# Kernel tuning notes

Hardware: AMD Instinct MI355X
Metric: run time of the kernel (lower is better)

Reference implementation:

```python
import jax, jax.numpy as jnp
import numpy as np

V, D, H, P = 50000, 128, 256, 50      # vocab, embed_dim, hidden, pos_dim
N, T = 2048, 50                        # total sentences, max words per sentence
NDOC, L = 64, 32                       # docs, sentences per doc (N = NDOC*L)
PDOC, PSENT = 50, 100                  # pos embedding table sizes


def _gru(x, Wi, Wh, bi, bh):
    """PyTorch-style GRU, batch_first. x: [B,T,Din] -> [B,T,H]."""
    B = x.shape[0]
    Hh = Wh.shape[1]
    xg = jnp.einsum('btd,gd->btg', x, Wi) + bi  # [B,T,3H] precomputed input gates

    def step(h, xg_t):
        hg = h @ Wh.T + bh
        xr, xz, xn = jnp.split(xg_t, 3, axis=-1)
        hr, hz, hn = jnp.split(hg, 3, axis=-1)
        r = jax.nn.sigmoid(xr + hr)
        z = jax.nn.sigmoid(xz + hz)
        n = jnp.tanh(xn + r * hn)
        hnew = (1.0 - z) * n + z * h
        return hnew, hnew

    h0 = jnp.zeros((B, Hh), x.dtype)
    _, hs = jax.lax.scan(step, h0, jnp.swapaxes(xg, 0, 1))
    return jnp.swapaxes(hs, 0, 1)


def _bigru(x, pf, pb):
    hf = _gru(x, *pf)
    hb = _gru(x[:, ::-1], *pb)[:, ::-1]
    return jnp.concatenate([hf, hb], axis=-1)


def _masked_max(h, lens):
    """Ragged max-pool over time: h [B,T,C], lens [B] -> [B,C]; zeros for len==0."""
    Tt = h.shape[1]
    mask = jnp.arange(Tt)[None, :, None] < lens[:, None, None]
    m = jnp.max(jnp.where(mask, h, -jnp.inf), axis=1)
    return jnp.where(lens[:, None] > 0, m, 0.0)


def setup_inputs() -> dict:
    key = jax.random.key(0)
    ks = iter(jax.random.split(key, 64))

    def w(shape, s=0.05):
        return jax.random.normal(next(ks), shape, jnp.float32) * s

    x = jax.random.randint(next(ks), (N, T), 1, V)          # no padding tokens
    doc_lens = jnp.full((NDOC,), L, dtype=jnp.int32)
    d = {'x': x, 'doc_lens': doc_lens, 'embed': w((V, D)).at[0].set(0.0)}
    for pre, din in (('w', D), ('s', 2 * H), ('d', 2 * H)):
        for suf in ('f', 'b'):
            d[f'{pre}Wi_{suf}'] = w((3 * H, din))
            d[f'{pre}Wh_{suf}'] = w((3 * H, H))
            d[f'{pre}bi_{suf}'] = w((3 * H,))
            d[f'{pre}bh_{suf}'] = w((3 * H,))
    d['doc_pos_tab'] = w((PDOC, P))
    d['sent_pos_tab'] = w((PSENT, P))
    d['w_content'] = w((2 * H,))
    d['W_sal'] = w((2 * H, 4 * H))
    d['w_dpos'] = w((P,))
    d['w_spos'] = w((P,))
    d['sent_bias'] = w((1,))
    return d


def reference(x, doc_lens, embed,
              wWi_f, wWh_f, wbi_f, wbh_f, wWi_b, wWh_b, wbi_b, wbh_b,
              sWi_f, sWh_f, sbi_f, sbh_f, sWi_b, sWh_b, sbi_b, sbh_b,
              dWi_f, dWh_f, dbi_f, dbh_f, dWi_b, dWh_b, dbi_b, dbh_b,
              doc_pos_tab, sent_pos_tab, w_content, W_sal, w_dpos, w_spos,
              sent_bias):
    sent_lens = jnp.sum(jnp.sign(x), axis=1)                 # [N]
    e = embed[x]                                             # [N,T,D]
    hw = _bigru(e, (wWi_f, wWh_f, wbi_f, wbh_f), (wWi_b, wWh_b, wbi_b, wbh_b))
    sent_vec = _masked_max(hw, sent_lens)                    # [N,2H]

    n_docs = doc_lens.shape[0]
    Ld = sent_vec.shape[0] // n_docs
    docs = sent_vec.reshape(n_docs, Ld, -1)                  # [nd,L,2H]
    hs = _bigru(docs, (sWi_f, sWh_f, sbi_f, sbh_f), (sWi_b, sWh_b, sbi_b, sbh_b))
    doc_vec = _masked_max(hs, doc_lens)                      # [nd,2H]

    hd = _bigru(doc_vec[None], (dWi_f, dWh_f, dbi_f, dbh_f),
                (dWi_b, dWh_b, dbi_b, dbh_b))[0]             # [nd,2H]
    blog_vec = jnp.max(hd, axis=0)                           # [2H]

    context = jnp.concatenate(
        [jnp.broadcast_to(blog_vec, (n_docs, blog_vec.shape[0])), doc_vec],
        axis=-1)                                             # [nd,4H]

    content = docs @ w_content                               # [nd,L]
    salience = jnp.einsum('nld,de,ne->nl', docs, W_sal, context)

    pdoc = doc_pos_tab.shape[0]
    psent = sent_pos_tab.shape[0]
    di = (jnp.arange(n_docs) * pdoc) // n_docs               # [nd]
    safe_lens = jnp.maximum(doc_lens, 1).astype(jnp.int32)
    si = (jnp.arange(Ld, dtype=jnp.int32)[None, :] * psent) // safe_lens[:, None]
    si = jnp.minimum(si, psent - 1)                          # [nd,L]
    dscore = doc_pos_tab[di] @ w_dpos                        # [nd]
    sscore = sent_pos_tab[si] @ w_spos                       # [nd,L]

    scores = content + salience + dscore[:, None] + sscore + sent_bias[0]
    return scores.reshape(-1)                                # [N]
```

## Files before the change

kernel.cpp:

```cpp
#include <hip/hip_runtime.h>
#include <math.h>

#define HID 256
#define G3 768
#define DIM 128
#define TW 50
#define NSENT 2048
#define NDOC 64
#define LSENT 32
#define PDOC 50
#define PSENT 100
#define PDIMM 50

using i32x4 = __attribute__((ext_vector_type(4))) int;

static constexpr long OFFB_W1F  = 0;
static constexpr long OFFB_W2F  = 294912;
static constexpr long OFFB_W1B  = 589824;
static constexpr long OFFB_W2B  = 884736;
static constexpr long OFFB_SW1F = 1179648;
static constexpr long OFFB_SW2F = 1376256;
static constexpr long OFFB_SW1B = 1572864;
static constexpr long OFFB_SW2B = 1769472;
static constexpr long OFFB_DW1F = 1966080;
static constexpr long OFFB_DW2F = 2162688;
static constexpr long OFFB_DW1B = 2359296;
static constexpr long OFFB_DW2B = 2555904;

static constexpr long OFF_W4_sWi_f = 688128;
static constexpr long OFF_W4_sWi_b = 1081344;
static constexpr long OFF_W4_dWi_f = 1474560;
static constexpr long OFF_W4_dWi_b = 1867776;
static constexpr long OFF_W4_salT  = 2260992;
static constexpr long OFF_LENS     = 2785280;
static constexpr long OFF_SENTVEC  = 2787328;
static constexpr long OFF_XGS      = 3835904;
static constexpr long OFF_DOCVEC   = 6981632;
static constexpr long OFF_XGD      = 7014400;
static constexpr long OFF_BLOG     = 7112704;

#define SW_Q (0.3f/127.0f)
#define SX_Q (1.0f/127.0f)

__device__ __forceinline__ float sigm(float v){ return 1.0f/(1.0f+__expf(-v)); }
__device__ __forceinline__ float tanhfast(float v){ return 1.0f - 2.0f/(1.0f+__expf(2.0f*v)); }

__device__ __forceinline__ void fma4(float& acc, const float4 a, const float4 b){
  acc = fmaf(a.x, b.x, fmaf(a.y, b.y, fmaf(a.z, b.z, fmaf(a.w, b.w, acc))));
}

__device__ __forceinline__ void quant2(float v, int& a, int& b){
  float q1 = rintf(fminf(fmaxf(v*127.0f, -127.0f), 127.0f));
  a = (int)q1;
  float resid = v - q1*(1.0f/127.0f);
  b = (int)rintf(fminf(fmaxf(resid*32512.0f, -127.0f), 127.0f));
}
__device__ __forceinline__ int pack4(int a0,int a1,int a2,int a3){
  return (a0&255) | ((a1&255)<<8) | ((a2&255)<<16) | ((a3&255)<<24);
}

__device__ __forceinline__ void mfma3(const signed char* __restrict__ W1,
                                      const signed char* __restrict__ W2, long fo,
                                      i32x4 x1v, i32x4 x2v, i32x4& p1, i32x4& p23){
  const i32x4 a1 = *(const i32x4*)(W1 + fo);
  const i32x4 a2 = *(const i32x4*)(W2 + fo);
  p1  = __builtin_amdgcn_mfma_i32_16x16x64_i8(a1, x1v, p1, 0,0,0);
  p23 = __builtin_amdgcn_mfma_i32_16x16x64_i8(a1, x2v, p23,0,0,0);
  p23 = __builtin_amdgcn_mfma_i32_16x16x64_i8(a2, x1v, p23,0,0,0);
}

struct PE { const float* Wh; const float* Wi; signed char* d1; signed char* d2; long cnt; int nkc; };
struct PP { PE e[6]; };
__global__ __launch_bounds__(256) void k_prep(PP pp, long total){
  long g = (long)blockIdx.x*256 + threadIdx.x;
  if (g >= total) return;
  int k = 0; long r = g;
  while (r >= pp.e[k].cnt) { r -= pp.e[k].cnt; ++k; }
  const float* Wh = pp.e[k].Wh;
  const float* Wi = pp.e[k].Wi;
  int span = pp.e[k].nkc << 10;
  int mt  = (int)(r / span);
  int rem = (int)(r % span);
  int kc  = rem >> 10;
  int l   = (rem >> 4) & 63;
  int e16 = rem & 15;
  int row = mt*16 + (l & 15);
  int kk  = kc*64 + ((e16>>2)*16 + (l>>4)*4 + (e16&3));
  float wv = (kk < 256) ? Wh[(long)row*256 + kk] : Wi[(long)row*128 + (kk-256)];
  float q1 = rintf(fminf(fmaxf(wv*(1.0f/SW_Q), -127.0f), 127.0f));
  float resid = wv - q1*SW_Q;
  float q2 = rintf(fminf(fmaxf(resid*(256.0f/SW_Q), -127.0f), 127.0f));
  pp.e[k].d1[r] = (signed char)(int)q1;
  pp.e[k].d2[r] = (signed char)(int)q2;
}

struct TD { const float* src; long dst; long cnt; int sh; int R; };
struct TT { TD t[5]; };

__global__ __launch_bounds__(256) void k_transpose(TT tt, float* __restrict__ ws, long total){
  long g = (long)blockIdx.x*256 + threadIdx.x;
  if (g >= total) return;
  int k = 0; long r = g;
  while (r >= tt.t[k].cnt) { r -= tt.t[k].cnt; ++k; }
  const float* src = tt.t[k].src;
  int sh = tt.t[k].sh; int R = tt.t[k].R;
  long j = r >> sh;
  int col = (int)(r & ((1L<<sh)-1));
  ws[tt.t[k].dst + (((long)(col>>2))*R + j)*4 + (col&3)] = src[r];
}

__global__ __launch_bounds__(256) void k_lens(const int* __restrict__ x, int* __restrict__ lens){
  int n = blockIdx.x*256 + threadIdx.x;
  if (n >= NSENT) return;
  int c = 0;
  for (int t = 0; t < TW; ++t) c += (x[n*TW + t] != 0) ? 1 : 0;
  lens[n] = c;
}

__global__ __launch_bounds__(1024, 4)
void k_word_i8(const int* __restrict__ x, const float* __restrict__ embed,
               const signed char* __restrict__ W1f, const signed char* __restrict__ W2f,
               const signed char* __restrict__ W1b, const signed char* __restrict__ W2b,
               const float* __restrict__ bi_f, const float* __restrict__ bi_b,
               const float* __restrict__ bh_f, const float* __restrict__ bh_b,
               const int* __restrict__ lens, float* __restrict__ sent_vec)
{
  __shared__ __align__(16) signed char X1[6*1024];
  __shared__ __align__(16) signed char X2[6*1024];
  const int blk = blockIdx.x;
  const int dir = blk & 1;
  const int n0  = (blk >> 1) * 16;
  const int tid = threadIdx.x;
  const int w    = tid >> 6;
  const int lane = tid & 63;
  const int hi4  = lane >> 4;
  const int s    = lane & 15;
  const int j0   = w*16 + hi4*4;
  const signed char* W1 = dir ? W1b : W1f;
  const signed char* W2 = dir ? W2b : W2f;
  const float* bi = dir ? bi_b : bi_f;
  const float* bh = dir ? bh_b : bh_f;

  float b_r[4], b_z[4], b_nx[4], b_nh[4];
  #pragma unroll
  for (int i = 0; i < 4; ++i) {
    int j = j0 + i;
    b_r[i]  = bi[j]     + bh[j];
    b_z[i]  = bi[j+256] + bh[j+256];
    b_nx[i] = bi[j+512];
    b_nh[i] = bh[j+512];
  }
  float hold[4] = {0.f,0.f,0.f,0.f};
  float rmax[4] = {-INFINITY,-INFINITY,-INFINITY,-INFINITY};
  const int len_s = lens[n0 + s];

  for (int i2 = tid; i2 < 1536; i2 += 1024) { ((int*)X1)[i2] = 0; ((int*)X2)[i2] = 0; }

  if (tid < 512) {
    const int tx = dir ? (TW-1) : 0;
    const int s2 = tid >> 5;
    const int d0 = (tid & 31) * 4;
    const int tok = x[(n0 + s2)*TW + tx];
    const float4 ev = *(const float4*)(embed + (long)tok*DIM + d0);
    int a0,a1,a2,a3,c0,c1v,c2v,c3;
    quant2(ev.x,a0,c0); quant2(ev.y,a1,c1v); quant2(ev.z,a2,c2v); quant2(ev.w,a3,c3);
    const int kc = 4 + (d0 >> 6);
    const int kk = d0 & 63;
    const int ee0 = (kk >> 4) << 2;
    const int lp  = ((kk >> 2) & 3)*16 + s2;
    const int off = kc*1024 + lp*16 + ee0;
    *(int*)(X1 + off) = pack4(a0,a1,a2,a3);
    *(int*)(X2 + off) = pack4(c0,c1v,c2v,c3);
  }
  __syncthreads();

  for (int t = 0; t < TW; ++t) {
    i32x4 p1r  = {0,0,0,0}, p23r  = {0,0,0,0};
    i32x4 p1z  = {0,0,0,0}, p23z  = {0,0,0,0};
    i32x4 p1nh = {0,0,0,0}, p23nh = {0,0,0,0};
    i32x4 p1nx = {0,0,0,0}, p23nx = {0,0,0,0};
    #pragma unroll
    for (int kc = 0; kc < 6; ++kc) {
      const i32x4 x1v = *(const i32x4*)(X1 + kc*1024 + lane*16);
      const i32x4 x2v = *(const i32x4*)(X2 + kc*1024 + lane*16);
      mfma3(W1, W2, ((long)(w*6      + kc))*1024 + lane*16, x1v, x2v, p1r, p23r);
      mfma3(W1, W2, ((long)((w+16)*6 + kc))*1024 + lane*16, x1v, x2v, p1z, p23z);
      if (kc < 4) mfma3(W1, W2, ((long)((w+32)*6 + kc))*1024 + lane*16, x1v, x2v, p1nh, p23nh);
      else        mfma3(W1, W2, ((long)((w+32)*6 + kc))*1024 + lane*16, x1v, x2v, p1nx, p23nx);
    }
    const float cc1 = SW_Q * SX_Q;
    const float cc2 = cc1 * (1.0f/256.0f);
    #pragma unroll
    for (int i = 0; i < 4; ++i) {
      float ar = fmaf(cc1, (float)p1r[i],  fmaf(cc2, (float)p23r[i],  b_r[i]));
      float az = fmaf(cc1, (float)p1z[i],  fmaf(cc2, (float)p23z[i],  b_z[i]));
      float ah = fmaf(cc1, (float)p1nh[i], fmaf(cc2, (float)p23nh[i], b_nh[i]));
      float ax = fmaf(cc1, (float)p1nx[i], fmaf(cc2, (float)p23nx[i], b_nx[i]));
      float rg = sigm(ar);
      float zg = sigm(az);
      float ng = tanhfast(ax + rg*ah);
      float hv = (1.0f - zg)*ng + zg*hold[i];
      hold[i] = hv;
      bool inm = dir ? (t >= TW - len_s) : (t < len_s);
      if (inm) rmax[i] = fmaxf(rmax[i], hv);
    }
    __syncthreads();
    {
      const int kcw = j0 >> 6;
      const int kk  = j0 & 63;
      const int ee0 = (kk >> 4) << 2;
      const int lp  = ((kk >> 2) & 3)*16 + s;
      const int off = kcw*1024 + lp*16 + ee0;
      int a0,a1,a2,a3,c0,c1v,c2v,c3;
      quant2(hold[0],a0,c0); quant2(hold[1],a1,c1v);
      quant2(hold[2],a2,c2v); quant2(hold[3],a3,c3);
      *(int*)(X1 + off) = pack4(a0,a1,a2,a3);
      *(int*)(X2 + off) = pack4(c0,c1v,c2v,c3);
    }
    if (t < TW-1 && tid < 512) {
      const int tx = dir ? (TW-2-t) : (t+1);
      const int s2 = tid >> 5;
      const int d0 = (tid & 31) * 4;
      const int tok = x[(n0 + s2)*TW + tx];
      const float4 ev = *(const float4*)(embed + (long)tok*DIM + d0);
      int a0,a1,a2,a3,c0,c1v,c2v,c3;
      quant2(ev.x,a0,c0); quant2(ev.y,a1,c1v); quant2(ev.z,a2,c2v); quant2(ev.w,a3,c3);
      const int kc = 4 + (d0 >> 6);
      const int kk = d0 & 63;
      const int ee0 = (kk >> 4) << 2;
      const int lp  = ((kk >> 2) & 3)*16 + s2;
      const int off = kc*1024 + lp*16 + ee0;
      *(int*)(X1 + off) = pack4(a0,a1,a2,a3);
      *(int*)(X2 + off) = pack4(c0,c1v,c2v,c3);
    }
    __syncthreads();
  }
  #pragma unroll
  for (int i = 0; i < 4; ++i) {
    float v = (len_s > 0) ? rmax[i] : 0.0f;
    sent_vec[(long)(n0+s)*(2*HID) + dir*HID + j0 + i] = v;
  }
}

__global__ __launch_bounds__(1024, 4)
void k_sent_i8(const float* __restrict__ xg,
               const signed char* __restrict__ SW1f, const signed char* __restrict__ SW2f,
               const signed char* __restrict__ SW1b, const signed char* __restrict__ SW2b,
               const float* __restrict__ bh_f, const float* __restrict__ bh_b,
               const int* __restrict__ dlens, float* __restrict__ doc_vec)
{
  __shared__ __align__(16) signed char X1[4*1024];
  __shared__ __align__(16) signed char X2[4*1024];
  const int blk = blockIdx.x;
  const int dir = blk & 1;
  const int g   = blk >> 1;
  const int tid = threadIdx.x;
  const int w    = tid >> 6;
  const int lane = tid & 63;
  const int hi4  = lane >> 4;
  const int s    = lane & 15;
  const int j0   = w*16 + hi4*4;
  const int d    = g*16 + s;
  const signed char* W1 = dir ? SW1b : SW1f;
  const signed char* W2 = dir ? SW2b : SW2f;
  const float* bh = dir ? bh_b : bh_f;
  float b_r[4], b_z[4], b_nh[4];
  #pragma unroll
  for (int i = 0; i < 4; ++i) {
    b_r[i]  = bh[j0+i];
    b_z[i]  = bh[j0+i+256];
    b_nh[i] = bh[j0+i+512];
  }
  float hold[4] = {0.f,0.f,0.f,0.f};
  float rmax[4] = {-INFINITY,-INFINITY,-INFINITY,-INFINITY};
  const int len_d = dlens[d];
  ((int*)X1)[tid] = 0; ((int*)X2)[tid] = 0;
  __syncthreads();

  for (int t = 0; t < LSENT; ++t) {
    const int row = dir ? (LSENT-1-t) : t;
    const float* xgr = xg + ((long)(d*LSENT + row))*1536 + dir*768;
    const float4 xr4 = *(const float4*)(xgr + j0);
    const float4 xz4 = *(const float4*)(xgr + 256 + j0);
    const float4 xn4 = *(const float4*)(xgr + 512 + j0);
    const float xr[4] = {xr4.x, xr4.y, xr4.z, xr4.w};
    const float xz[4] = {xz4.x, xz4.y, xz4.z, xz4.w};
    const float xn[4] = {xn4.x, xn4.y, xn4.z, xn4.w};
    i32x4 p1r = {0,0,0,0}, p23r = {0,0,0,0};
    i32x4 p1z = {0,0,0,0}, p23z = {0,0,0,0};
    i32x4 p1n = {0,0,0,0}, p23n = {0,0,0,0};
    #pragma unroll
    for (int kc = 0; kc < 4; ++kc) {
      const i32x4 x1v = *(const i32x4*)(X1 + kc*1024 + lane*16);
      const i32x4 x2v = *(const i32x4*)(X2 + kc*1024 + lane*16);
      mfma3(W1, W2, ((long)(w*4      + kc))*1024 + lane*16, x1v, x2v, p1r, p23r);
      mfma3(W1, W2, ((long)((w+16)*4 + kc))*1024 + lane*16, x1v, x2v, p1z, p23z);
      mfma3(W1, W2, ((long)((w+32)*4 + kc))*1024 + lane*16, x1v, x2v, p1n, p23n);
    }
    const float cc1 = SW_Q * SX_Q;
    const float cc2 = cc1 * (1.0f/256.0f);
    #pragma unroll
    for (int i = 0; i < 4; ++i) {
      float ar = xr[i] + fmaf(cc1, (float)p1r[i], fmaf(cc2, (float)p23r[i], b_r[i]));
      float az = xz[i] + fmaf(cc1, (float)p1z[i], fmaf(cc2, (float)p23z[i], b_z[i]));
      float ah =         fmaf(cc1, (float)p1n[i], fmaf(cc2, (float)p23n[i], b_nh[i]));
      float rg = sigm(ar);
      float zg = sigm(az);
      float ng = tanhfast(xn[i] + rg*ah);
      float hv = (1.0f - zg)*ng + zg*hold[i];
      hold[i] = hv;
      bool inm = dir ? (t >= LSENT - len_d) : (t < len_d);
      if (inm) rmax[i] = fmaxf(rmax[i], hv);
    }
    __syncthreads();
    {
      const int kcw = j0 >> 6;
      const int kk  = j0 & 63;
      const int ee0 = (kk >> 4) << 2;
      const int lp  = ((kk >> 2) & 3)*16 + s;
      const int off = kcw*1024 + lp*16 + ee0;
      int a0,a1,a2,a3,c0,c1v,c2v,c3;
      quant2(hold[0],a0,c0); quant2(hold[1],a1,c1v);
      quant2(hold[2],a2,c2v); quant2(hold[3],a3,c3);
      *(int*)(X1 + off) = pack4(a0,a1,a2,a3);
      *(int*)(X2 + off) = pack4(c0,c1v,c2v,c3);
    }
    __syncthreads();
  }
  #pragma unroll
  for (int i = 0; i < 4; ++i)
    doc_vec[(long)d*512 + dir*256 + j0 + i] = (len_d > 0) ? rmax[i] : 0.0f;
}

__global__ __launch_bounds__(1024, 4)
void k_doc_i8(const float* __restrict__ xg,
              const signed char* __restrict__ DW1f, const signed char* __restrict__ DW2f,
              const signed char* __restrict__ DW1b, const signed char* __restrict__ DW2b,
              const float* __restrict__ bh_f, const float* __restrict__ bh_b,
              float* __restrict__ blog)
{
  __shared__ __align__(16) signed char X1[4*1024];
  __shared__ __align__(16) signed char X2[4*1024];
  const int dir = blockIdx.x;
  const int tid = threadIdx.x;
  const int w    = tid >> 6;
  const int lane = tid & 63;
  const int hi4  = lane >> 4;
  const int s    = lane & 15;
  const int j0   = w*16 + hi4*4;
  const signed char* W1 = dir ? DW1b : DW1f;
  const signed char* W2 = dir ? DW2b : DW2f;
  const float* bh = dir ? bh_b : bh_f;
  float b_r[4], b_z[4], b_nh[4];
  #pragma unroll
  for (int i = 0; i < 4; ++i) {
    b_r[i]  = bh[j0+i];
    b_z[i]  = bh[j0+i+256];
    b_nh[i] = bh[j0+i+512];
  }
  float hold[4] = {0.f,0.f,0.f,0.f};
  float rmax[4] = {-INFINITY,-INFINITY,-INFINITY,-INFINITY};
  ((int*)X1)[tid] = 0; ((int*)X2)[tid] = 0;
  __syncthreads();

  for (int t = 0; t < NDOC; ++t) {
    const int row = dir ? (NDOC-1-t) : t;
    const float* xgr = xg + (long)row*1536 + dir*768;
    const float4 xr4 = *(const float4*)(xgr + j0);
    const float4 xz4 = *(const float4*)(xgr + 256 + j0);
    const float4 xn4 = *(const float4*)(xgr + 512 + j0);
    const float xr[4] = {xr4.x, xr4.y, xr4.z, xr4.w};
    const float xz[4] = {xz4.x, xz4.y, xz4.z, xz4.w};
    const float xn[4] = {xn4.x, xn4.y, xn4.z, xn4.w};
    i32x4 p1r = {0,0,0,0}, p23r = {0,0,0,0};
    i32x4 p1z = {0,0,0,0}, p23z = {0,0,0,0};
    i32x4 p1n = {0,0,0,0}, p23n = {0,0,0,0};
    #pragma unroll
    for (int kc = 0; kc < 4; ++kc) {
      const i32x4 x1v = *(const i32x4*)(X1 + kc*1024 + lane*16);
      const i32x4 x2v = *(const i32x4*)(X2 + kc*1024 + lane*16);
      mfma3(W1, W2, ((long)(w*4      + kc))*1024 + lane*16, x1v, x2v, p1r, p23r);
      mfma3(W1, W2, ((long)((w+16)*4 + kc))*1024 + lane*16, x1v, x2v, p1z, p23z);
      mfma3(W1, W2, ((long)((w+32)*4 + kc))*1024 + lane*16, x1v, x2v, p1n, p23n);
    }
    const float cc1 = SW_Q * SX_Q;
    const float cc2 = cc1 * (1.0f/256.0f);
    #pragma unroll
    for (int i = 0; i < 4; ++i) {
      float ar = xr[i] + fmaf(cc1, (float)p1r[i], fmaf(cc2, (float)p23r[i], b_r[i]));
      float az = xz[i] + fmaf(cc1, (float)p1z[i], fmaf(cc2, (float)p23z[i], b_z[i]));
      float ah =         fmaf(cc1, (float)p1n[i], fmaf(cc2, (float)p23n[i], b_nh[i]));
      float rg = sigm(ar);
      float zg = sigm(az);
      float ng = tanhfast(xn[i] + rg*ah);
      float hv = (1.0f - zg)*ng + zg*hold[i];
      hold[i] = hv;
      rmax[i] = fmaxf(rmax[i], hv);
    }
    __syncthreads();
    if (s == 0) {
      const int kcw = j0 >> 6;
      const int kk  = j0 & 63;
      const int ee0 = (kk >> 4) << 2;
      const int lp  = ((kk >> 2) & 3)*16;
      const int off = kcw*1024 + lp*16 + ee0;
      int a0,a1,a2,a3,c0,c1v,c2v,c3;
      quant2(hold[0],a0,c0); quant2(hold[1],a1,c1v);
      quant2(hold[2],a2,c2v); quant2(hold[3],a3,c3);
      *(int*)(X1 + off) = pack4(a0,a1,a2,a3);
      *(int*)(X2 + off) = pack4(c0,c1v,c2v,c3);
    }
    __syncthreads();
  }
  if (s == 0) {
    #pragma unroll
    for (int i = 0; i < 4; ++i) blog[dir*256 + j0 + i] = rmax[i];
  }
}

__global__ __launch_bounds__(256)
void k_gates(const float* __restrict__ A,
             const float* __restrict__ W4f, const float* __restrict__ W4b,
             const float* __restrict__ bif, const float* __restrict__ bib,
             float* __restrict__ out)
{
  __shared__ __align__(16) float a_lds[8][512];
  const int r0 = blockIdx.x * 8;
  const int j  = threadIdx.x;
  #pragma unroll
  for (int q = 0; q < 4; ++q) {
    int fi = j + q*256;
    int rr = fi >> 7; int cc = (fi & 127) * 4;
    *(float4*)(&a_lds[rr][cc]) = *(const float4*)(A + (long)(r0+rr)*512 + cc);
  }
  __syncthreads();
  float acc[6][8];
  {
    float bias[6] = { bif[j], bif[j+256], bif[j+512], bib[j], bib[j+256], bib[j+512] };
    #pragma unroll
    for (int k = 0; k < 6; ++k)
      #pragma unroll
      for (int rr = 0; rr < 8; ++rr) acc[k][rr] = bias[k];
  }
  for (int d4 = 0; d4 < 128; ++d4) {
    float4 w0 = *(const float4*)(W4f + ((long)d4*G3 + j      )*4);
    float4 w1 = *(const float4*)(W4f + ((long)d4*G3 + j + 256)*4);
    float4 w2 = *(const float4*)(W4f + ((long)d4*G3 + j + 512)*4);
    float4 w3 = *(const float4*)(W4b + ((long)d4*G3 + j      )*4);
    float4 w4v= *(const float4*)(W4b + ((long)d4*G3 + j + 256)*4);
    float4 w5 = *(const float4*)(W4b + ((long)d4*G3 + j + 512)*4);
    #pragma unroll
    for (int rr = 0; rr < 8; ++rr){
      const float4 a4 = *(const float4*)(&a_lds[rr][d4*4]);
      fma4(acc[0][rr], w0, a4);
      fma4(acc[1][rr], w1, a4);
      fma4(acc[2][rr], w2, a4);
      fma4(acc[3][rr], w3, a4);
      fma4(acc[4][rr], w4v, a4);
      fma4(acc[5][rr], w5, a4);
    }
  }
  #pragma unroll
  for (int rr = 0; rr < 8; ++rr){
    long base = (long)(r0+rr)*1536;
    out[base + j      ] = acc[0][rr];
    out[base + j + 256] = acc[1][rr];
    out[base + j + 512] = acc[2][rr];
    out[base + j + 768] = acc[3][rr];
    out[base + j +1024] = acc[4][rr];
    out[base + j +1280] = acc[5][rr];
  }
}

__global__ __launch_bounds__(256)
void k_score(const float* __restrict__ docs , const float* __restrict__ doc_vec,
             const float* __restrict__ blog, const float* __restrict__ W4sal,
             const float* __restrict__ w_content, const float* __restrict__ w_dpos,
             const float* __restrict__ w_spos, const float* __restrict__ doc_pos_tab,
             const float* __restrict__ sent_pos_tab, const float* __restrict__ sent_bias,
             const int* __restrict__ dlens, float* __restrict__ out)
{
  __shared__ __align__(16) float ctx[1024];
  __shared__ __align__(16) float cw[1024];
  const int n = blockIdx.x;
  const int j = threadIdx.x;
  ctx[j]       = blog[j];
  ctx[256 + j] = blog[256 + j];
  ctx[512 + j] = doc_vec[(long)n*512 + j];
  ctx[768 + j] = doc_vec[(long)n*512 + 256 + j];
  cw[512 + j]  = w_content[j];
  cw[768 + j]  = w_content[256 + j];
  __syncthreads();
  float acc0 = 0.0f, acc1 = 0.0f;
  for (int e4 = 0; e4 < 256; ++e4) {
    const float4 c4 = *(const float4*)(&ctx[e4*4]);
    const float4 w0 = *(const float4*)(W4sal + ((long)e4*512 + j      )*4);
    const float4 w1 = *(const float4*)(W4sal + ((long)e4*512 + j + 256)*4);
    fma4(acc0, w0, c4);
    fma4(acc1, w1, c4);
  }
  cw[j] = acc0; cw[j + 256] = acc1;
  __syncthreads();
  const int l = j >> 3, p = j & 7;
  const float* drow = docs + ((long)n*LSENT + l)*512;
  float pc = 0.0f, ps = 0.0f;
  for (int i = p*64; i < p*64 + 64; i += 4) {
    const float4 dv  = *(const float4*)(drow + i);
    const float4 wc4 = *(const float4*)(&cw[512 + i]);
    const float4 cp4 = *(const float4*)(&cw[i]);
    fma4(pc, dv, wc4);
    fma4(ps, dv, cp4);
  }
  #pragma unroll
  for (int o = 1; o < 8; o <<= 1) {
    pc += __shfl_xor(pc, o, 8);
    ps += __shfl_xor(ps, o, 8);
  }
  if (p == 0) {
    const int dlen = dlens[n];
    const int di = (n * PDOC) / NDOC;
    float ds = 0.0f;
    for (int i = 0; i < PDIMM; ++i) ds = fmaf(doc_pos_tab[(long)di*PDIMM + i], w_dpos[i], ds);
    const int safe = (dlen > 1) ? dlen : 1;
    int si = (l * PSENT) / safe;
    if (si > PSENT-1) si = PSENT-1;
    float ss = 0.0f;
    for (int i = 0; i < PDIMM; ++i) ss = fmaf(sent_pos_tab[(long)si*PDIMM + i], w_spos[i], ss);
    out[n*LSENT + l] = pc + ps + ds + ss + sent_bias[0];
  }
}

extern "C" void kernel_launch(void* const* d_in, const int* in_sizes, int n_in,
                              void* d_out, int out_size, void* d_ws, size_t ws_size,
                              hipStream_t stream)
{
  const int*   x        = (const int*)  d_in[0];
  const int*   doc_lens = (const int*)  d_in[1];
  const float* embed    = (const float*)d_in[2];
  const float* wWi_f = (const float*)d_in[3];
  const float* wWh_f = (const float*)d_in[4];
  const float* wbi_f = (const float*)d_in[5];
  const float* wbh_f = (const float*)d_in[6];
  const float* wWi_b = (const float*)d_in[7];
  const float* wWh_b = (const float*)d_in[8];
  const float* wbi_b = (const float*)d_in[9];
  const float* wbh_b = (const float*)d_in[10];
  const float* sWi_f = (const float*)d_in[11];
  const float* sWh_f = (const float*)d_in[12];
  const float* sbi_f = (const float*)d_in[13];
  const float* sbh_f = (const float*)d_in[14];
  const float* sWi_b = (const float*)d_in[15];
  const float* sWh_b = (const float*)d_in[16];
  const float* sbi_b = (const float*)d_in[17];
  const float* sbh_b = (const float*)d_in[18];
  const float* dWi_f = (const float*)d_in[19];
  const float* dWh_f = (const float*)d_in[20];
  const float* dbi_f = (const float*)d_in[21];
  const float* dbh_f = (const float*)d_in[22];
  const float* dWi_b = (const float*)d_in[23];
  const float* dWh_b = (const float*)d_in[24];
  const float* dbi_b = (const float*)d_in[25];
  const float* dbh_b = (const float*)d_in[26];
  const float* doc_pos_tab  = (const float*)d_in[27];
  const float* sent_pos_tab = (const float*)d_in[28];
  const float* w_content    = (const float*)d_in[29];
  const float* W_sal        = (const float*)d_in[30];
  const float* w_dpos       = (const float*)d_in[31];
  const float* w_spos       = (const float*)d_in[32];
  const float* sent_bias    = (const float*)d_in[33];

  float* ws = (float*)d_ws;
  signed char* wsb = (signed char*)d_ws;

  PP pp;
  auto setp = [&](int i, const float* Wh, const float* Wi, long d1, long d2, long cnt, int nkc){
    pp.e[i].Wh = Wh; pp.e[i].Wi = Wi; pp.e[i].d1 = wsb + d1; pp.e[i].d2 = wsb + d2;
    pp.e[i].cnt = cnt; pp.e[i].nkc = nkc;
  };
  setp(0, wWh_f, wWi_f, OFFB_W1F,  OFFB_W2F,  294912, 6);
  setp(1, wWh_b, wWi_b, OFFB_W1B,  OFFB_W2B,  294912, 6);
  setp(2, sWh_f, sWh_f, OFFB_SW1F, OFFB_SW2F, 196608, 4);
  setp(3, sWh_b, sWh_b, OFFB_SW1B, OFFB_SW2B, 196608, 4);
  setp(4, dWh_f, dWh_f, OFFB_DW1F, OFFB_DW2F, 196608, 4);
  setp(5, dWh_b, dWh_b, OFFB_DW1B, OFFB_DW2B, 196608, 4);
  long ptotal = 2*294912 + 4*196608;
  k_prep<<<(int)((ptotal + 255)/256), 256, 0, stream>>>(pp, ptotal);

  TT tt;
  int idx = 0;
  auto add = [&](const float* src, long dst, int R, int Dk, int sh){
    tt.t[idx].src = src; tt.t[idx].dst = dst; tt.t[idx].cnt = (long)R*Dk;
    tt.t[idx].sh = sh; tt.t[idx].R = R; ++idx;
  };
  add(sWi_f, OFF_W4_sWi_f, 768, 512, 9);
  add(sWi_b, OFF_W4_sWi_b, 768, 512, 9);
  add(dWi_f, OFF_W4_dWi_f, 768, 512, 9);
  add(dWi_b, OFF_W4_dWi_b, 768, 512, 9);
  add(W_sal, OFF_W4_salT,  512, 1024, 10);
  long total = 0;
  for (int i = 0; i < 5; ++i) total += tt.t[i].cnt;
  k_transpose<<<(int)((total + 255)/256), 256, 0, stream>>>(tt, ws, total);
  k_lens<<<NSENT/256, 256, 0, stream>>>(x, (int*)(ws + OFF_LENS));

  k_word_i8<<<256, 1024, 0, stream>>>(x, embed,
      wsb + OFFB_W1F, wsb + OFFB_W2F, wsb + OFFB_W1B, wsb + OFFB_W2B,
      wbi_f, wbi_b, wbh_f, wbh_b,
      (const int*)(ws + OFF_LENS), ws + OFF_SENTVEC);

  k_gates<<<NSENT/8, 256, 0, stream>>>(ws + OFF_SENTVEC,
      ws + OFF_W4_sWi_f, ws + OFF_W4_sWi_b, sbi_f, sbi_b, ws + OFF_XGS);

  k_sent_i8<<<8, 1024, 0, stream>>>(ws + OFF_XGS,
      wsb + OFFB_SW1F, wsb + OFFB_SW2F, wsb + OFFB_SW1B, wsb + OFFB_SW2B,
      sbh_f, sbh_b, doc_lens, ws + OFF_DOCVEC);

  k_gates<<<NDOC/8, 256, 0, stream>>>(ws + OFF_DOCVEC,
      ws + OFF_W4_dWi_f, ws + OFF_W4_dWi_b, dbi_f, dbi_b, ws + OFF_XGD);

  k_doc_i8<<<2, 1024, 0, stream>>>(ws + OFF_XGD,
      wsb + OFFB_DW1F, wsb + OFFB_DW2F, wsb + OFFB_DW1B, wsb + OFFB_DW2B,
      dbh_f, dbh_b, ws + OFF_BLOG);

  k_score<<<NDOC, 256, 0, stream>>>(ws + OFF_SENTVEC, ws + OFF_DOCVEC, ws + OFF_BLOG,
      ws + OFF_W4_salT, w_content, w_dpos, w_spos,
      doc_pos_tab, sent_pos_tab, sent_bias, doc_lens, (float*)d_out);
}
```

Before: 1.753 ms.

## Process two sentence tiles per word-GRU block and prefetch recurrent weights

The word-level GRU kernel now handles 32 sentences per block as two 16-row tiles. Each int8 weight fragment loaded from global memory feeds MFMAs for both tiles, halving weight traffic per sentence and halving the grid to 128 blocks. Biases move to shared memory to free registers. The sentence- and doc-level GRU kernels software-prefetch the next k-chunk's weight fragments into registers, and the gates GEMM kernel doubles rows per block to 16 for more weight reuse. In exchange, register pressure rises and the word kernel runs fewer blocks, which may lower occupancy.

```diff
diff --git a/kernel.cpp b/kernel.cpp
--- a/kernel.cpp
+++ b/kernel.cpp
@@ -59,14 +59,13 @@
   return (a0&255) | ((a1&255)<<8) | ((a2&255)<<16) | ((a3&255)<<24);
 }
 
-__device__ __forceinline__ void mfma3(const signed char* __restrict__ W1,
-                                      const signed char* __restrict__ W2, long fo,
-                                      i32x4 x1v, i32x4 x2v, i32x4& p1, i32x4& p23){
-  const i32x4 a1 = *(const i32x4*)(W1 + fo);
-  const i32x4 a2 = *(const i32x4*)(W2 + fo);
-  p1  = __builtin_amdgcn_mfma_i32_16x16x64_i8(a1, x1v, p1, 0,0,0);
-  p23 = __builtin_amdgcn_mfma_i32_16x16x64_i8(a1, x2v, p23,0,0,0);
-  p23 = __builtin_amdgcn_mfma_i32_16x16x64_i8(a2, x1v, p23,0,0,0);
+#define MFMA_I8(a,b,c) __builtin_amdgcn_mfma_i32_16x16x64_i8((a),(b),(c),0,0,0)
+
+__device__ __forceinline__ void mfma3r(i32x4 a1, i32x4 a2, i32x4 x1, i32x4 x2,
+                                       i32x4& p1, i32x4& p23){
+  p1  = MFMA_I8(a1, x1, p1);
+  p23 = MFMA_I8(a1, x2, p23);
+  p23 = MFMA_I8(a2, x1, p23);
 }
 
 struct PE { const float* Wh; const float* Wi; signed char* d1; signed char* d2; long cnt; int nkc; };
@@ -125,11 +124,12 @@
                const float* __restrict__ bh_f, const float* __restrict__ bh_b,
                const int* __restrict__ lens, float* __restrict__ sent_vec)
 {
-  __shared__ __align__(16) signed char X1[6*1024];
-  __shared__ __align__(16) signed char X2[6*1024];
+  __shared__ __align__(16) signed char X1[2][6*1024];
+  __shared__ __align__(16) signed char X2[2][6*1024];
+  __shared__ float bR[256], bZ[256], bNX[256], bNH[256];
   const int blk = blockIdx.x;
   const int dir = blk & 1;
-  const int n0  = (blk >> 1) * 16;
+  const int n0  = (blk >> 1) * 32;
   const int tid = threadIdx.x;
   const int w    = tid >> 6;
   const int lane = tid & 63;
@@ -141,69 +141,112 @@
   const float* bi = dir ? bi_b : bi_f;
   const float* bh = dir ? bh_b : bh_f;
 
-  float b_r[4], b_z[4], b_nx[4], b_nh[4];
-  #pragma unroll
-  for (int i = 0; i < 4; ++i) {
-    int j = j0 + i;
-    b_r[i]  = bi[j]     + bh[j];
-    b_z[i]  = bi[j+256] + bh[j+256];
-    b_nx[i] = bi[j+512];
-    b_nh[i] = bh[j+512];
-  }
-  float hold[4] = {0.f,0.f,0.f,0.f};
-  float rmax[4] = {-INFINITY,-INFINITY,-INFINITY,-INFINITY};
-  const int len_s = lens[n0 + s];
-
-  for (int i2 = tid; i2 < 1536; i2 += 1024) { ((int*)X1)[i2] = 0; ((int*)X2)[i2] = 0; }
-
-  if (tid < 512) {
+  if (tid < 256) {
+    bR[tid]  = bi[tid]     + bh[tid];
+    bZ[tid]  = bi[tid+256] + bh[tid+256];
+    bNX[tid] = bi[tid+512];
+    bNH[tid] = bh[tid+512];
+  }
+
+  float hold[2][4] = {{0.f,0.f,0.f,0.f},{0.f,0.f,0.f,0.f}};
+  float rmax[2][4];
+  #pragma unroll
+  for (int p = 0; p < 2; ++p)
+    #pragma unroll
+    for (int i = 0; i < 4; ++i) rmax[p][i] = -INFINITY;
+  int len_[2];
+  len_[0] = lens[n0 + s];
+  len_[1] = lens[n0 + 16 + s];
+
+  {
+    const int p  = tid >> 9;
+    const int ii = tid & 511;
+    ((int*)(X1[p]))[ii]       = 0;
+    ((int*)(X1[p]))[ii + 512] = 0;
+    ((int*)(X2[p]))[ii]       = 0;
+    ((int*)(X2[p]))[ii + 512] = 0;
+  }
+
+  const int s2g = tid >> 5;
+  const int pg  = s2g >> 4;
+  const int spg = s2g & 15;
+  const int d0g = (tid & 31) * 4;
+  const int kcg = 4 + (d0g >> 6);
+  const int offg = kcg*1024 + (((d0g & 63) >> 2 & 3)*16 + spg)*16 + (((d0g & 63) >> 4) << 2);
+  {
     const int tx = dir ? (TW-1) : 0;
-    const int s2 = tid >> 5;
-    const int d0 = (tid & 31) * 4;
-    const int tok = x[(n0 + s2)*TW + tx];
-    const float4 ev = *(const float4*)(embed + (long)tok*DIM + d0);
+    const int tok = x[(n0 + s2g)*TW + tx];
+    const float4 ev = *(const float4*)(embed + (long)tok*DIM + d0g);
     int a0,a1,a2,a3,c0,c1v,c2v,c3;
     quant2(ev.x,a0,c0); quant2(ev.y,a1,c1v); quant2(ev.z,a2,c2v); quant2(ev.w,a3,c3);
-    const int kc = 4 + (d0 >> 6);
-    const int kk = d0 & 63;
-    const int ee0 = (kk >> 4) << 2;
-    const int lp  = ((kk >> 2) & 3)*16 + s2;
-    const int off = kc*1024 + lp*16 + ee0;
-    *(int*)(X1 + off) = pack4(a0,a1,a2,a3);
-    *(int*)(X2 + off) = pack4(c0,c1v,c2v,c3);
+    *(int*)(X1[pg] + offg) = pack4(a0,a1,a2,a3);
+    *(int*)(X2[pg] + offg) = pack4(c0,c1v,c2v,c3);
   }
   __syncthreads();
 
   for (int t = 0; t < TW; ++t) {
-    i32x4 p1r  = {0,0,0,0}, p23r  = {0,0,0,0};
-    i32x4 p1z  = {0,0,0,0}, p23z  = {0,0,0,0};
-    i32x4 p1nh = {0,0,0,0}, p23nh = {0,0,0,0};
-    i32x4 p1nx = {0,0,0,0}, p23nx = {0,0,0,0};
+    i32x4 p1r[2], p23r[2], p1z[2], p23z[2], p1nh[2], p23nh[2], p1nx[2], p23nx[2];
+    #pragma unroll
+    for (int p = 0; p < 2; ++p) {
+      p1r[p] = i32x4{0,0,0,0};  p23r[p] = i32x4{0,0,0,0};
+      p1z[p] = i32x4{0,0,0,0};  p23z[p] = i32x4{0,0,0,0};
+      p1nh[p]= i32x4{0,0,0,0};  p23nh[p]= i32x4{0,0,0,0};
+      p1nx[p]= i32x4{0,0,0,0};  p23nx[p]= i32x4{0,0,0,0};
+    }
     #pragma unroll
     for (int kc = 0; kc < 6; ++kc) {
-      const i32x4 x1v = *(const i32x4*)(X1 + kc*1024 + lane*16);
-      const i32x4 x2v = *(const i32x4*)(X2 + kc*1024 + lane*16);
-      mfma3(W1, W2, ((long)(w*6      + kc))*1024 + lane*16, x1v, x2v, p1r, p23r);
-      mfma3(W1, W2, ((long)((w+16)*6 + kc))*1024 + lane*16, x1v, x2v, p1z, p23z);
-      if (kc < 4) mfma3(W1, W2, ((long)((w+32)*6 + kc))*1024 + lane*16, x1v, x2v, p1nh, p23nh);
-      else        mfma3(W1, W2, ((long)((w+32)*6 + kc))*1024 + lane*16, x1v, x2v, p1nx, p23nx);
+      const i32x4 xa1 = *(const i32x4*)(X1[0] + kc*1024 + lane*16);
+      const i32x4 xa2 = *(const i32x4*)(X2[0] + kc*1024 + lane*16);
+      const i32x4 xb1 = *(const i32x4*)(X1[1] + kc*1024 + lane*16);
+      const i32x4 xb2 = *(const i32x4*)(X2[1] + kc*1024 + lane*16);
+      const long o0 = ((long)(w*6      + kc))*1024 + lane*16;
+      const long o1 = ((long)((w+16)*6 + kc))*1024 + lane*16;
+      const long o2 = ((long)((w+32)*6 + kc))*1024 + lane*16;
+      {
+        const i32x4 f0 = *(const i32x4*)(W1 + o0);
+        const i32x4 f1 = *(const i32x4*)(W1 + o1);
+        const i32x4 f2 = *(const i32x4*)(W1 + o2);
+        p1r[0] = MFMA_I8(f0, xa1, p1r[0]);  p23r[0] = MFMA_I8(f0, xa2, p23r[0]);
+        p1r[1] = MFMA_I8(f0, xb1, p1r[1]);  p23r[1] = MFMA_I8(f0, xb2, p23r[1]);
+        p1z[0] = MFMA_I8(f1, xa1, p1z[0]);  p23z[0] = MFMA_I8(f1, xa2, p23z[0]);
+        p1z[1] = MFMA_I8(f1, xb1, p1z[1]);  p23z[1] = MFMA_I8(f1, xb2, p23z[1]);
+        if (kc < 4) {
+          p1nh[0] = MFMA_I8(f2, xa1, p1nh[0]);  p23nh[0] = MFMA_I8(f2, xa2, p23nh[0]);
+          p1nh[1] = MFMA_I8(f2, xb1, p1nh[1]);  p23nh[1] = MFMA_I8(f2, xb2, p23nh[1]);
+        } else {
+          p1nx[0] = MFMA_I8(f2, xa1, p1nx[0]);  p23nx[0] = MFMA_I8(f2, xa2, p23nx[0]);
+          p1nx[1] = MFMA_I8(f2, xb1, p1nx[1]);  p23nx[1] = MFMA_I8(f2, xb2, p23nx[1]);
+        }
+      }
+      {
+        const i32x4 g0 = *(const i32x4*)(W2 + o0);
+        const i32x4 g1 = *(const i32x4*)(W2 + o1);
+        const i32x4 g2 = *(const i32x4*)(W2 + o2);
+        p23r[0] = MFMA_I8(g0, xa1, p23r[0]);  p23r[1] = MFMA_I8(g0, xb1, p23r[1]);
+        p23z[0] = MFMA_I8(g1, xa1, p23z[0]);  p23z[1] = MFMA_I8(g1, xb1, p23z[1]);
+        if (kc < 4) { p23nh[0] = MFMA_I8(g2, xa1, p23nh[0]);  p23nh[1] = MFMA_I8(g2, xb1, p23nh[1]); }
+        else        { p23nx[0] = MFMA_I8(g2, xa1, p23nx[0]);  p23nx[1] = MFMA_I8(g2, xb1, p23nx[1]); }
+      }
     }
     const float cc1 = SW_Q * SX_Q;
     const float cc2 = cc1 * (1.0f/256.0f);
     #pragma unroll
-    for (int i = 0; i < 4; ++i) {
-      float ar = fmaf(cc1, (float)p1r[i],  fmaf(cc2, (float)p23r[i],  b_r[i]));
-      float az = fmaf(cc1, (float)p1z[i],  fmaf(cc2, (float)p23z[i],  b_z[i]));
-      float ah = fmaf(cc1, (float)p1nh[i], fmaf(cc2, (float)p23nh[i], b_nh[i]));
-      float ax = fmaf(cc1, (float)p1nx[i], fmaf(cc2, (float)p23nx[i], b_nx[i]));
-      float rg = sigm(ar);
-      float zg = sigm(az);
-      float ng = tanhfast(ax + rg*ah);
-      float hv = (1.0f - zg)*ng + zg*hold[i];
-      hold[i] = hv;
-      bool inm = dir ? (t >= TW - len_s) : (t < len_s);
-      if (inm) rmax[i] = fmaxf(rmax[i], hv);
-    }
+    for (int p = 0; p < 2; ++p)
+      #pragma unroll
+      for (int i = 0; i < 4; ++i) {
+        const int jj = j0 + i;
+        float ar = fmaf(cc1, (float)p1r[p][i],  fmaf(cc2, (float)p23r[p][i],  bR[jj]));
+        float az = fmaf(cc1, (float)p1z[p][i],  fmaf(cc2, (float)p23z[p][i],  bZ[jj]));
+        float ah = fmaf(cc1, (float)p1nh[p][i], fmaf(cc2, (float)p23nh[p][i], bNH[jj]));
+        float ax = fmaf(cc1, (float)p1nx[p][i], fmaf(cc2, (float)p23nx[p][i], bNX[jj]));
+        float rg = sigm(ar);
+        float zg = sigm(az);
+        float ng = tanhfast(ax + rg*ah);
+        float hv = (1.0f - zg)*ng + zg*hold[p][i];
+        hold[p][i] = hv;
+        bool inm = dir ? (t >= TW - len_[p]) : (t < len_[p]);
+        if (inm) rmax[p][i] = fmaxf(rmax[p][i], hv);
+      }
     __syncthreads();
     {
       const int kcw = j0 >> 6;
@@ -211,35 +254,33 @@
       const int ee0 = (kk >> 4) << 2;
       const int lp  = ((kk >> 2) & 3)*16 + s;
       const int off = kcw*1024 + lp*16 + ee0;
-      int a0,a1,a2,a3,c0,c1v,c2v,c3;
-      quant2(hold[0],a0,c0); quant2(hold[1],a1,c1v);
-      quant2(hold[2],a2,c2v); quant2(hold[3],a3,c3);
-      *(int*)(X1 + off) = pack4(a0,a1,a2,a3);
-      *(int*)(X2 + off) = pack4(c0,c1v,c2v,c3);
-    }
-    if (t < TW-1 && tid < 512) {
+      #pragma unroll
+      for (int p = 0; p < 2; ++p) {
+        int a0,a1,a2,a3,c0,c1v,c2v,c3;
+        quant2(hold[p][0],a0,c0); quant2(hold[p][1],a1,c1v);
+        quant2(hold[p][2],a2,c2v); quant2(hold[p][3],a3,c3);
+        *(int*)(X1[p] + off) = pack4(a0,a1,a2,a3);
+        *(int*)(X2[p] + off) = pack4(c0,c1v,c2v,c3);
+      }
+    }
+    if (t < TW-1) {
       const int tx = dir ? (TW-2-t) : (t+1);
-      const int s2 = tid >> 5;
-      const int d0 = (tid & 31) * 4;
-      const int tok = x[(n0 + s2)*TW + tx];
-      const float4 ev = *(const float4*)(embed + (long)tok*DIM + d0);
+      const int tok = x[(n0 + s2g)*TW + tx];
+      const float4 ev = *(const float4*)(embed + (long)tok*DIM + d0g);
       int a0,a1,a2,a3,c0,c1v,c2v,c3;
       quant2(ev.x,a0,c0); quant2(ev.y,a1,c1v); quant2(ev.z,a2,c2v); quant2(ev.w,a3,c3);
-      const int kc = 4 + (d0 >> 6);
-      const int kk = d0 & 63;
-      const int ee0 = (kk >> 4) << 2;
-      const int lp  = ((kk >> 2) & 3)*16 + s2;
-      const int off = kc*1024 + lp*16 + ee0;
-      *(int*)(X1 + off) = pack4(a0,a1,a2,a3);
-      *(int*)(X2 + off) = pack4(c0,c1v,c2v,c3);
+      *(int*)(X1[pg] + offg) = pack4(a0,a1,a2,a3);
+      *(int*)(X2[pg] + offg) = pack4(c0,c1v,c2v,c3);
     }
     __syncthreads();
   }
   #pragma unroll
-  for (int i = 0; i < 4; ++i) {
-    float v = (len_s > 0) ? rmax[i] : 0.0f;
-    sent_vec[(long)(n0+s)*(2*HID) + dir*HID + j0 + i] = v;
-  }
+  for (int p = 0; p < 2; ++p)
+    #pragma unroll
+    for (int i = 0; i < 4; ++i) {
+      float v = (len_[p] > 0) ? rmax[p][i] : 0.0f;
+      sent_vec[(long)(n0 + p*16 + s)*(2*HID) + dir*HID + j0 + i] = v;
+    }
 }
 
 __global__ __launch_bounds__(1024, 4)
@@ -277,6 +318,14 @@
   ((int*)X1)[tid] = 0; ((int*)X2)[tid] = 0;
   __syncthreads();
 
+  i32x4 a1b[2][3], a2b[2][3];
+  #pragma unroll
+  for (int m = 0; m < 3; ++m) {
+    const long fo = ((long)((w + m*16)*4))*1024 + lane*16;
+    a1b[0][m] = *(const i32x4*)(W1 + fo);
+    a2b[0][m] = *(const i32x4*)(W2 + fo);
+  }
+
   for (int t = 0; t < LSENT; ++t) {
     const int row = dir ? (LSENT-1-t) : t;
     const float* xgr = xg + ((long)(d*LSENT + row))*1536 + dir*768;
@@ -291,11 +340,20 @@
     i32x4 p1n = {0,0,0,0}, p23n = {0,0,0,0};
     #pragma unroll
     for (int kc = 0; kc < 4; ++kc) {
+      const int cur = kc & 1;
+      const int nxt = cur ^ 1;
+      const int kcn = (kc + 1) & 3;
+      #pragma unroll
+      for (int m = 0; m < 3; ++m) {
+        const long fo = ((long)((w + m*16)*4 + kcn))*1024 + lane*16;
+        a1b[nxt][m] = *(const i32x4*)(W1 + fo);
+        a2b[nxt][m] = *(const i32x4*)(W2 + fo);
+      }
       const i32x4 x1v = *(const i32x4*)(X1 + kc*1024 + lane*16);
       const i32x4 x2v = *(const i32x4*)(X2 + kc*1024 + lane*16);
-      mfma3(W1, W2, ((long)(w*4      + kc))*1024 + lane*16, x1v, x2v, p1r, p23r);
-      mfma3(W1, W2, ((long)((w+16)*4 + kc))*1024 + lane*16, x1v, x2v, p1z, p23z);
-      mfma3(W1, W2, ((long)((w+32)*4 + kc))*1024 + lane*16, x1v, x2v, p1n, p23n);
+      mfma3r(a1b[cur][0], a2b[cur][0], x1v, x2v, p1r, p23r);
+      mfma3r(a1b[cur][1], a2b[cur][1], x1v, x2v, p1z, p23z);
+      mfma3r(a1b[cur][2], a2b[cur][2], x1v, x2v, p1n, p23n);
     }
     const float cc1 = SW_Q * SX_Q;
     const float cc2 = cc1 * (1.0f/256.0f);
@@ -363,6 +421,14 @@
   ((int*)X1)[tid] = 0; ((int*)X2)[tid] = 0;
   __syncthreads();
 
+  i32x4 a1b[2][3], a2b[2][3];
+  #pragma unroll
+  for (int m = 0; m < 3; ++m) {
+    const long fo = ((long)((w + m*16)*4))*1024 + lane*16;
+    a1b[0][m] = *(const i32x4*)(W1 + fo);
+    a2b[0][m] = *(const i32x4*)(W2 + fo);
+  }
+
   for (int t = 0; t < NDOC; ++t) {
     const int row = dir ? (NDOC-1-t) : t;
     const float* xgr = xg + (long)row*1536 + dir*768;
@@ -377,11 +443,20 @@
     i32x4 p1n = {0,0,0,0}, p23n = {0,0,0,0};
     #pragma unroll
     for (int kc = 0; kc < 4; ++kc) {
+      const int cur = kc & 1;
+      const int nxt = cur ^ 1;
+      const int kcn = (kc + 1) & 3;
+      #pragma unroll
+      for (int m = 0; m < 3; ++m) {
+        const long fo = ((long)((w + m*16)*4 + kcn))*1024 + lane*16;
+        a1b[nxt][m] = *(const i32x4*)(W1 + fo);
+        a2b[nxt][m] = *(const i32x4*)(W2 + fo);
+      }
       const i32x4 x1v = *(const i32x4*)(X1 + kc*1024 + lane*16);
       const i32x4 x2v = *(const i32x4*)(X2 + kc*1024 + lane*16);
-      mfma3(W1, W2, ((long)(w*4      + kc))*1024 + lane*16, x1v, x2v, p1r, p23r);
-      mfma3(W1, W2, ((long)((w+16)*4 + kc))*1024 + lane*16, x1v, x2v, p1z, p23z);
-      mfma3(W1, W2, ((long)((w+32)*4 + kc))*1024 + lane*16, x1v, x2v, p1n, p23n);
+      mfma3r(a1b[cur][0], a2b[cur][0], x1v, x2v, p1r, p23r);
+      mfma3r(a1b[cur][1], a2b[cur][1], x1v, x2v, p1z, p23z);
+      mfma3r(a1b[cur][2], a2b[cur][2], x1v, x2v, p1n, p23n);
     }
     const float cc1 = SW_Q * SX_Q;
     const float cc2 = cc1 * (1.0f/256.0f);
@@ -424,23 +499,23 @@
              const float* __restrict__ bif, const float* __restrict__ bib,
              float* __restrict__ out)
 {
-  __shared__ __align__(16) float a_lds[8][512];
-  const int r0 = blockIdx.x * 8;
+  __shared__ __align__(16) float a_lds[16][512];
+  const int r0 = blockIdx.x * 16;
   const int j  = threadIdx.x;
   #pragma unroll
-  for (int q = 0; q < 4; ++q) {
+  for (int q = 0; q < 8; ++q) {
     int fi = j + q*256;
     int rr = fi >> 7; int cc = (fi & 127) * 4;
     *(float4*)(&a_lds[rr][cc]) = *(const float4*)(A + (long)(r0+rr)*512 + cc);
   }
   __syncthreads();
-  float acc[6][8];
+  float acc[6][16];
   {
     float bias[6] = { bif[j], bif[j+256], bif[j+512], bib[j], bib[j+256], bib[j+512] };
     #pragma unroll
     for (int k = 0; k < 6; ++k)
       #pragma unroll
-      for (int rr = 0; rr < 8; ++rr) acc[k][rr] = bias[k];
+      for (int rr = 0; rr < 16; ++rr) acc[k][rr] = bias[k];
   }
   for (int d4 = 0; d4 < 128; ++d4) {
     float4 w0 = *(const float4*)(W4f + ((long)d4*G3 + j      )*4);
@@ -450,7 +525,7 @@
     float4 w4v= *(const float4*)(W4b + ((long)d4*G3 + j + 256)*4);
     float4 w5 = *(const float4*)(W4b + ((long)d4*G3 + j + 512)*4);
     #pragma unroll
-    for (int rr = 0; rr < 8; ++rr){
+    for (int rr = 0; rr < 16; ++rr){
       const float4 a4 = *(const float4*)(&a_lds[rr][d4*4]);
       fma4(acc[0][rr], w0, a4);
       fma4(acc[1][rr], w1, a4);
@@ -461,7 +536,7 @@
     }
   }
   #pragma unroll
-  for (int rr = 0; rr < 8; ++rr){
+  for (int rr = 0; rr < 16; ++rr){
     long base = (long)(r0+rr)*1536;
     out[base + j      ] = acc[0][rr];
     out[base + j + 256] = acc[1][rr];
@@ -602,19 +677,19 @@
   k_transpose<<<(int)((total + 255)/256), 256, 0, stream>>>(tt, ws, total);
   k_lens<<<NSENT/256, 256, 0, stream>>>(x, (int*)(ws + OFF_LENS));
 
-  k_word_i8<<<256, 1024, 0, stream>>>(x, embed,
+  k_word_i8<<<128, 1024, 0, stream>>>(x, embed,
       wsb + OFFB_W1F, wsb + OFFB_W2F, wsb + OFFB_W1B, wsb + OFFB_W2B,
       wbi_f, wbi_b, wbh_f, wbh_b,
       (const int*)(ws + OFF_LENS), ws + OFF_SENTVEC);
 
-  k_gates<<<NSENT/8, 256, 0, stream>>>(ws + OFF_SENTVEC,
+  k_gates<<<NSENT/16, 256, 0, stream>>>(ws + OFF_SENTVEC,
       ws + OFF_W4_sWi_f, ws + OFF_W4_sWi_b, sbi_f, sbi_b, ws + OFF_XGS);
 
   k_sent_i8<<<8, 1024, 0, stream>>>(ws + OFF_XGS,
       wsb + OFFB_SW1F, wsb + OFFB_SW2F, wsb + OFFB_SW1B, wsb + OFFB_SW2B,
       sbh_f, sbh_b, doc_lens, ws + OFF_DOCVEC);
 
-  k_gates<<<NDOC/8, 256, 0, stream>>>(ws + OFF_DOCVEC,
+  k_gates<<<NDOC/16, 256, 0, stream>>>(ws + OFF_DOCVEC,
       ws + OFF_W4_dWi_f, ws + OFF_W4_dWi_b, dbi_f, dbi_b, ws + OFF_XGD);
 
   k_doc_i8<<<2, 1024, 0, stream>>>(ws + OFF_XGD,
```

After: 2.194 ms. 1.25x slower.
